# Kernel optimization log

Hardware: AMD Instinct MI355X
Metric: run time of the kernel (lower is better)

The kernel has to match this reference:

```python
import jax, jax.numpy as jnp
import numpy as np

H, HKV, HD = 16, 4, 128
EPS = 1.1920928955078125e-07  # float32 eps, torch F.rms_norm default


def _rms_norm(t):
    return t * jax.lax.rsqrt(jnp.mean(t * t, axis=-1, keepdims=True) + EPS)


def _rope(t, cos, sin):
    # t: [B, T, h, HD]; cos/sin: [T, HD//2] -> broadcast [1, T, 1, HD//2]
    te, to = t[..., 0::2], t[..., 1::2]
    c = cos[None, :, None, :]
    s = sin[None, :, None, :]
    re = te * c - to * s
    ro = te * s + to * c
    return jnp.stack((re, ro), axis=-1).reshape(t.shape)


def setup_inputs() -> dict:
    key = jax.random.key(0)
    ks = jax.random.split(key, 5)
    B, T, C = 2, 2048, 2048
    return {
        "x": jax.random.normal(ks[0], (B, T, C), jnp.float32),
        "Wq": jax.random.normal(ks[1], (C, C), jnp.float32) * 0.02,
        "Wk": jax.random.normal(ks[2], (HKV * HD, C), jnp.float32) * 0.02,
        "Wv": jax.random.normal(ks[3], (HKV * HD, C), jnp.float32) * 0.02,
        "Wo": jax.random.normal(ks[4], (C, C), jnp.float32) * 0.02,
        "q_gain": jnp.full((H,), 5.0, jnp.float32),
    }


def reference(x, Wq, Wk, Wv, Wo, q_gain):
    B, T, C = x.shape
    q = (x @ Wq.T).reshape(B, T, H, HD)
    k = (x @ Wk.T).reshape(B, T, HKV, HD)
    v = (x @ Wv.T).reshape(B, T, HKV, HD)

    q = _rms_norm(q)
    k = _rms_norm(k)

    theta = 1.0 / (10000.0 ** (jnp.arange(0, HD, 2, dtype=jnp.float32) / HD))
    t = jnp.arange(T, dtype=jnp.float32)
    freqs = jnp.outer(t, theta)  # [T, HD//2]
    cos, sin = jnp.cos(freqs), jnp.sin(freqs)

    q = _rope(q, cos, sin)
    k = _rope(k, cos, sin)
    q = q * q_gain[None, None, :, None]

    qh = q.transpose(0, 2, 1, 3)                       # [B, H, T, HD]
    kh = jnp.repeat(k.transpose(0, 2, 1, 3), H // HKV, axis=1)
    vh = jnp.repeat(v.transpose(0, 2, 1, 3), H // HKV, axis=1)

    scale = 1.0 / jnp.sqrt(jnp.float32(HD))
    scores = jnp.einsum("bhqd,bhkd->bhqk", qh, kh) * scale
    causal = jnp.tril(jnp.ones((T, T), bool))
    scores = jnp.where(causal[None, None], scores, jnp.finfo(scores.dtype).min)
    attn = jax.nn.softmax(scores, axis=-1)
    out = jnp.einsum("bhqk,bhkd->bhqd", attn, vh)
    out = out.transpose(0, 2, 1, 3).reshape(B, T, C)
    return out @ Wo.T
```

## Files before the change

kernel.cpp:

```cpp
#include <hip/hip_runtime.h>
#include <hip/hip_bf16.h>

#define TSEQ 2048
#define CDIM 2048
#define NH   16
#define NKV  4
#define HDIM 128
#define BATCH 2
#define MROWS (BATCH*TSEQ)
#define KVC   (NKV*HDIM)
#define QKVC  (CDIM + 2*KVC)

typedef short bf16x8 __attribute__((ext_vector_type(8)));
typedef float f32x4  __attribute__((ext_vector_type(4)));

typedef const __attribute__((address_space(1))) void* gptr_t;
typedef __attribute__((address_space(3))) void* sptr_t;

__device__ inline void async16(const __hip_bfloat16* g, __hip_bfloat16* l) {
  __builtin_amdgcn_global_load_lds((gptr_t)g, (sptr_t)l, 16, 0, 0);
}

__device__ inline f32x4 mfma16(bf16x8 a, bf16x8 b, f32x4 c) {
  return __builtin_amdgcn_mfma_f32_16x16x32_bf16(a, b, c, 0, 0, 0);
}

__device__ inline float bfbits2f(unsigned short u) {
  return __uint_as_float(((unsigned)u) << 16);
}

__device__ inline unsigned short f2bfu(float x) {
  __hip_bfloat16 t = __float2bfloat16(x);
  return *(unsigned short*)&t;
}

__device__ inline int swz128(int row, int col) {
  return row*128 + (((col >> 3) ^ (row & 15)) << 3) + (col & 7);
}
__device__ inline int swz64(int row, int col) {
  return row*64 + ((((col >> 3) ^ row) & 7) << 3) + (col & 7);
}

__global__ void canary(const void* __restrict__ x, int* __restrict__ flag) {
  __shared__ int cnt[256];
  int tid = threadIdx.x;
  const unsigned short* u = (const unsigned short*)x;
  int c = 0;
#pragma unroll
  for (int i = 0; i < 4; ++i) {
    float a = fabsf(bfbits2f(u[(tid*4 + i)*2]));
    if (a >= 1e-6f && a <= 1e3f) c++;
  }
  cnt[tid] = c;
  __syncthreads();
  for (int s = 128; s > 0; s >>= 1) {
    if (tid < s) cnt[tid] += cnt[tid + s];
    __syncthreads();
  }
  if (tid == 0) *flag = (cnt[0] > 512) ? 1 : 0;
}

__global__ __launch_bounds__(256) void canonize_all(
    const void* __restrict__ xs,  const void* __restrict__ wqs,
    const void* __restrict__ wks, const void* __restrict__ wvs,
    const void* __restrict__ wos, const void* __restrict__ gs,
    __hip_bfloat16* __restrict__ xd,
    __hip_bfloat16* __restrict__ wqkv,
    __hip_bfloat16* __restrict__ wod,
    __hip_bfloat16* __restrict__ gd,
    const int* __restrict__ flag)
{
  int blk = blockIdx.x;
  const void* src; __hip_bfloat16* dst; int base, n;
  if      (blk < 4096) { src = xs;  dst = xd;                base = blk;        n = MROWS*CDIM; }
  else if (blk < 6144) { src = wqs; dst = wqkv;              base = blk - 4096; n = CDIM*CDIM; }
  else if (blk < 6656) { src = wks; dst = wqkv + (size_t)CDIM*CDIM;            base = blk - 6144; n = KVC*CDIM; }
  else if (blk < 7168) { src = wvs; dst = wqkv + (size_t)(CDIM+KVC)*CDIM;      base = blk - 6656; n = KVC*CDIM; }
  else if (blk < 9216) { src = wos; dst = wod;               base = blk - 7168; n = CDIM*CDIM; }
  else                 { src = gs;  dst = gd;                base = 0;          n = NH; }
  int idx = base*2048 + threadIdx.x*8;
  if (idx >= n) return;
  if (*flag) {
    *(bf16x8*)&dst[idx] = *(const bf16x8*)((const __hip_bfloat16*)src + idx);
  } else {
    const float* s = (const float*)src + idx;
#pragma unroll
    for (int j = 0; j < 8; ++j) dst[idx + j] = __float2bfloat16(s[j]);
  }
}

#define BK 64

__global__ __launch_bounds__(512, 2) void gemm_bt256(
    const __hip_bfloat16* __restrict__ A,
    const __hip_bfloat16* __restrict__ B,
    __hip_bfloat16* __restrict__ C,
    int M, int N, int K, int lda)
{
  __shared__ __align__(16) __hip_bfloat16 As[2][256*BK];
  __shared__ __align__(16) __hip_bfloat16 Bs[2][192*BK];
  const int tid  = threadIdx.x;
  const int wave = tid >> 6;
  const int lane = tid & 63;
  const int qd   = lane >> 4;
  const int ln   = lane & 15;
  const int m0   = blockIdx.y * 256;
  const int n0   = blockIdx.x * 192;
  const int wm   = (wave >> 2) * 128;
  const int wn   = (wave & 3) * 48;

  auto stageA = [&](int buf, int kt) {
    const __hip_bfloat16* src = A + (size_t)m0*lda + kt*BK;
    __hip_bfloat16* dst = &As[buf][0];
#pragma unroll
    for (int i = 0; i < 4; ++i) {
      int c = i*512 + tid;
      int row = c >> 3, sl = c & 7;
      int gs = sl ^ (row & 7);
      async16(&src[(size_t)row*lda + gs*8], &dst[(i*512 + wave*64)*8]);
    }
  };
  auto stageB = [&](int buf, int kt) {
    const __hip_bfloat16* src = B + (size_t)n0*K + kt*BK;
    __hip_bfloat16* dst = &Bs[buf][0];
#pragma unroll
    for (int i = 0; i < 3; ++i) {
      int c = i*512 + tid;
      int row = c >> 3, sl = c & 7;
      int gs = sl ^ (row & 7);
      async16(&src[(size_t)row*K + gs*8], &dst[(i*512 + wave*64)*8]);
    }
  };
  auto ldA = [&](int buf, int m, int kk) -> bf16x8 {
    int row = wm + m*16 + ln;
    return *(const bf16x8*)&As[buf][row*BK + (((kk*4 + qd) ^ (row & 7)) << 3)];
  };
  auto ldB = [&](int buf, int n, int kk) -> bf16x8 {
    int row = wn + n*16 + ln;
    return *(const bf16x8*)&Bs[buf][row*BK + (((kk*4 + qd) ^ (row & 7)) << 3)];
  };

  f32x4 acc[8][3] = {};
  const int nt = K / BK;

  stageA(0, 0); stageB(0, 0);
  if (nt > 1) {
    stageA(1, 1); stageB(1, 1);
    asm volatile("s_waitcnt vmcnt(7)" ::: "memory");
  } else {
    asm volatile("s_waitcnt vmcnt(0)" ::: "memory");
  }
  __builtin_amdgcn_s_barrier();

#pragma unroll 1
  for (int t = 0; t < nt; ++t) {
    const int buf = t & 1;
    bf16x8 a03[4][2], a47[4][2], b01[2][2], b2[2];

#pragma unroll
    for (int m = 0; m < 4; ++m)
#pragma unroll
      for (int kk = 0; kk < 2; ++kk) a03[m][kk] = ldA(buf, m, kk);
#pragma unroll
    for (int n = 0; n < 2; ++n)
#pragma unroll
      for (int kk = 0; kk < 2; ++kk) b01[n][kk] = ldB(buf, n, kk);
    __builtin_amdgcn_s_setprio(1);
#pragma unroll
    for (int m = 0; m < 4; ++m)
#pragma unroll
      for (int n = 0; n < 2; ++n)
#pragma unroll
        for (int kk = 0; kk < 2; ++kk)
          acc[m][n] = mfma16(a03[m][kk], b01[n][kk], acc[m][n]);
    __builtin_amdgcn_s_setprio(0);
    __builtin_amdgcn_s_barrier();

#pragma unroll
    for (int m = 0; m < 4; ++m)
#pragma unroll
      for (int kk = 0; kk < 2; ++kk) a47[m][kk] = ldA(buf, 4 + m, kk);
    __builtin_amdgcn_s_setprio(1);
#pragma unroll
    for (int m = 0; m < 4; ++m)
#pragma unroll
      for (int n = 0; n < 2; ++n)
#pragma unroll
        for (int kk = 0; kk < 2; ++kk)
          acc[4 + m][n] = mfma16(a47[m][kk], b01[n][kk], acc[4 + m][n]);
    __builtin_amdgcn_s_setprio(0);
    __builtin_amdgcn_s_barrier();

#pragma unroll
    for (int kk = 0; kk < 2; ++kk) b2[kk] = ldB(buf, 2, kk);
    if (t + 2 < nt) stageA(buf, t + 2);
    __builtin_amdgcn_s_setprio(1);
#pragma unroll
    for (int m = 0; m < 4; ++m)
#pragma unroll
      for (int kk = 0; kk < 2; ++kk)
        acc[m][2] = mfma16(a03[m][kk], b2[kk], acc[m][2]);
    __builtin_amdgcn_s_setprio(0);
    __builtin_amdgcn_s_barrier();

    if (t + 2 < nt) stageB(buf, t + 2);
    __builtin_amdgcn_s_setprio(1);
#pragma unroll
    for (int m = 0; m < 4; ++m)
#pragma unroll
      for (int kk = 0; kk < 2; ++kk)
        acc[4 + m][2] = mfma16(a47[m][kk], b2[kk], acc[4 + m][2]);
    __builtin_amdgcn_s_setprio(0);
    if (t + 2 < nt) asm volatile("s_waitcnt vmcnt(7)" ::: "memory");
    else            asm volatile("s_waitcnt vmcnt(0)" ::: "memory");
    __builtin_amdgcn_s_barrier();
  }

#pragma unroll
  for (int m = 0; m < 8; ++m)
#pragma unroll
    for (int n = 0; n < 3; ++n) {
      int row = m0 + wm + m*16 + qd*4;
      int col = n0 + wn + n*16 + ln;
#pragma unroll
      for (int r = 0; r < 4; ++r)
        C[(size_t)(row + r)*N + col] = __float2bfloat16(acc[m][n][r]);
    }
}

__global__ __launch_bounds__(512, 2) void gemm_out(
    const __hip_bfloat16* __restrict__ A,
    const __hip_bfloat16* __restrict__ B,
    void* __restrict__ C,
    int M, int N, int K, int lda, const int* __restrict__ flag)
{
  __shared__ __align__(16) __hip_bfloat16 As[2][128*BK];
  __shared__ __align__(16) __hip_bfloat16 Bs[2][256*BK];
  const int tid  = threadIdx.x;
  const int wave = tid >> 6;
  const int lane = tid & 63;
  const int qd   = lane >> 4;
  const int ln   = lane & 15;
  const int m0   = blockIdx.y * 128;
  const int n0   = blockIdx.x * 256;
  const int wm   = (wave >> 2) * 64;
  const int wn   = (wave & 3) * 64;

  auto stageA = [&](int buf, int kt) {
    const __hip_bfloat16* src = A + (size_t)m0*lda + kt*BK;
    __hip_bfloat16* dst = &As[buf][0];
#pragma unroll
    for (int i = 0; i < 2; ++i) {
      int c = i*512 + tid;
      int row = c >> 3, sl = c & 7;
      int gs = sl ^ (row & 7);
      async16(&src[(size_t)row*lda + gs*8], &dst[(i*512 + wave*64)*8]);
    }
  };
  auto stageB = [&](int buf, int kt) {
    const __hip_bfloat16* src = B + (size_t)n0*K + kt*BK;
    __hip_bfloat16* dst = &Bs[buf][0];
#pragma unroll
    for (int i = 0; i < 4; ++i) {
      int c = i*512 + tid;
      int row = c >> 3, sl = c & 7;
      int gs = sl ^ (row & 7);
      async16(&src[(size_t)row*K + gs*8], &dst[(i*512 + wave*64)*8]);
    }
  };
  auto ldA = [&](int buf, int m, int kk) -> bf16x8 {
    int row = wm + m*16 + ln;
    return *(const bf16x8*)&As[buf][row*BK + (((kk*4 + qd) ^ (row & 7)) << 3)];
  };
  auto ldB = [&](int buf, int n, int kk) -> bf16x8 {
    int row = wn + n*16 + ln;
    return *(const bf16x8*)&Bs[buf][row*BK + (((kk*4 + qd) ^ (row & 7)) << 3)];
  };

  f32x4 acc[4][4] = {};
  const int nt = K / BK;

  stageA(0, 0); stageB(0, 0);
  if (nt > 1) {
    stageA(1, 1); stageB(1, 1);
    asm volatile("s_waitcnt vmcnt(6)" ::: "memory");
  } else {
    asm volatile("s_waitcnt vmcnt(0)" ::: "memory");
  }
  __builtin_amdgcn_s_barrier();

#pragma unroll 1
  for (int t = 0; t < nt; ++t) {
    const int buf = t & 1;
    bf16x8 a01[2][2], a23[2][2], b01[2][2], b23[2][2];

#pragma unroll
    for (int m = 0; m < 2; ++m)
#pragma unroll
      for (int kk = 0; kk < 2; ++kk) a01[m][kk] = ldA(buf, m, kk);
#pragma unroll
    for (int n = 0; n < 2; ++n)
#pragma unroll
      for (int kk = 0; kk < 2; ++kk) b01[n][kk] = ldB(buf, n, kk);
    __builtin_amdgcn_s_setprio(1);
#pragma unroll
    for (int m = 0; m < 2; ++m)
#pragma unroll
      for (int n = 0; n < 2; ++n)
#pragma unroll
        for (int kk = 0; kk < 2; ++kk)
          acc[m][n] = mfma16(a01[m][kk], b01[n][kk], acc[m][n]);
    __builtin_amdgcn_s_setprio(0);
    __builtin_amdgcn_s_barrier();

#pragma unroll
    for (int m = 0; m < 2; ++m)
#pragma unroll
      for (int kk = 0; kk < 2; ++kk) a23[m][kk] = ldA(buf, 2 + m, kk);
    __builtin_amdgcn_s_setprio(1);
#pragma unroll
    for (int m = 0; m < 2; ++m)
#pragma unroll
      for (int n = 0; n < 2; ++n)
#pragma unroll
        for (int kk = 0; kk < 2; ++kk)
          acc[2 + m][n] = mfma16(a23[m][kk], b01[n][kk], acc[2 + m][n]);
    __builtin_amdgcn_s_setprio(0);
    __builtin_amdgcn_s_barrier();

#pragma unroll
    for (int n = 0; n < 2; ++n)
#pragma unroll
      for (int kk = 0; kk < 2; ++kk) b23[n][kk] = ldB(buf, 2 + n, kk);
    if (t + 2 < nt) stageA(buf, t + 2);
    __builtin_amdgcn_s_setprio(1);
#pragma unroll
    for (int m = 0; m < 2; ++m)
#pragma unroll
      for (int n = 0; n < 2; ++n)
#pragma unroll
        for (int kk = 0; kk < 2; ++kk)
          acc[m][2 + n] = mfma16(a01[m][kk], b23[n][kk], acc[m][2 + n]);
    __builtin_amdgcn_s_setprio(0);
    __builtin_amdgcn_s_barrier();

    if (t + 2 < nt) stageB(buf, t + 2);
    __builtin_amdgcn_s_setprio(1);
#pragma unroll
    for (int m = 0; m < 2; ++m)
#pragma unroll
      for (int n = 0; n < 2; ++n)
#pragma unroll
        for (int kk = 0; kk < 2; ++kk)
          acc[2 + m][2 + n] = mfma16(a23[m][kk], b23[n][kk], acc[2 + m][2 + n]);
    __builtin_amdgcn_s_setprio(0);
    if (t + 2 < nt) asm volatile("s_waitcnt vmcnt(6)" ::: "memory");
    else            asm volatile("s_waitcnt vmcnt(0)" ::: "memory");
    __builtin_amdgcn_s_barrier();
  }

  const bool isbf = (*flag != 0);
#pragma unroll
  for (int m = 0; m < 4; ++m)
#pragma unroll
    for (int n = 0; n < 4; ++n) {
      int row = m0 + wm + m*16 + qd*4;
      int col = n0 + wn + n*16 + ln;
#pragma unroll
      for (int r = 0; r < 4; ++r) {
        if (isbf) ((__hip_bfloat16*)C)[(size_t)(row + r)*N + col] = __float2bfloat16(acc[m][n][r]);
        else      ((float*)C)[(size_t)(row + r)*N + col] = acc[m][n][r];
      }
    }
}

__global__ __launch_bounds__(256) void prep_qk(
    __hip_bfloat16* __restrict__ qkv,
    const __hip_bfloat16* __restrict__ gain)
{
  int wid  = blockIdx.x * 4 + (threadIdx.x >> 6);
  int lane = threadIdx.x & 63;
  bool isq = wid < MROWS*NH;
  int m, h;
  __hip_bfloat16* p;
  if (isq) { m = wid >> 4; h = wid & 15; p = qkv + (size_t)m*QKVC + h*HDIM; }
  else     { int w2 = wid - MROWS*NH; m = w2 >> 2; h = w2 & 3; p = qkv + (size_t)m*QKVC + CDIM + h*HDIM; }

  ushort2 raw = *(const ushort2*)((const unsigned short*)p + 2*lane);
  float e = bfbits2f(raw.x), o = bfbits2f(raw.y);
  float ss = e*e + o*o;
#pragma unroll
  for (int off = 32; off >= 1; off >>= 1) ss += __shfl_xor(ss, off);
  float rms = rsqrtf(ss * (1.0f/128.0f) + 1.1920928955078125e-07f);
  e *= rms; o *= rms;

  float theta = exp2f(-(float)(2*lane) * (1.0f/128.0f) * 13.287712379549449f);
  int t = m & (TSEQ-1);
  float fr = (float)t * theta;
  float c = cosf(fr), s = sinf(fr);
  float re = e*c - o*s;
  float ro = e*s + o*c;

  if (isq) {
    float g = bfbits2f(*(const unsigned short*)&gain[h]) * 0.08838834764831845f;
    re *= g; ro *= g;
  }
  p[2*lane]   = __float2bfloat16(re);
  p[2*lane+1] = __float2bfloat16(ro);
}

__global__ __launch_bounds__(256) void transpose_v(
    const __hip_bfloat16* __restrict__ qkv, __hip_bfloat16* __restrict__ vt)
{
  __shared__ __hip_bfloat16 tile[32][34];
  int tx = threadIdx.x & 31;
  int ty = threadIdx.x >> 5;
  int r0 = blockIdx.x * 32;
  int c0 = blockIdx.y * 32;
#pragma unroll
  for (int i = 0; i < 4; ++i)
    tile[ty + i*8][tx] = qkv[(size_t)(r0 + ty + i*8)*QKVC + (CDIM + KVC) + c0 + tx];
  __syncthreads();
  int b = r0 >> 11;
  int t = r0 & (TSEQ-1);
  int hk = c0 >> 7;
  int d0 = c0 & (HDIM-1);
#pragma unroll
  for (int i = 0; i < 4; ++i) {
    int d = d0 + ty + i*8;
    vt[((size_t)((b*NKV + hk)*HDIM + d))*TSEQ + t + tx] = tile[tx][ty + i*8];
  }
}

__global__ __launch_bounds__(256, 2) void attn_kernel(
    const __hip_bfloat16* __restrict__ qkv,
    const __hip_bfloat16* __restrict__ vt,
    __hip_bfloat16* __restrict__ out)
{
  const int tid  = threadIdx.x;
  const int wave = tid >> 6;
  const int lane = tid & 63;
  const int qd = lane >> 4, ln = lane & 15;
  const int p  = blockIdx.x;
  const int h  = blockIdx.y;
  const int b  = blockIdx.z;
  const int hk = h >> 2;

  const __hip_bfloat16* K = qkv + (size_t)(b*TSEQ)*QKVC + CDIM + hk*HDIM;
  const __hip_bfloat16* V = vt + ((size_t)(b*NKV + hk)*HDIM)*TSEQ;

  __shared__ __align__(16) __hip_bfloat16 Ks[64*128];
  __shared__ __align__(16) __hip_bfloat16 Vs[128*64];
  __shared__ __align__(16) __hip_bfloat16 Pb[64*64];
  __shared__ float Lb[4][64];

  auto issueK = [&](int t0) {
#pragma unroll
    for (int i = 0; i < 4; ++i) {
      int c = i*256 + tid;
      int row = c >> 4, cc = c & 15;
      int gcc = cc ^ (row & 15);
      async16(&K[(size_t)(t0 + row)*QKVC + gcc*8], &Ks[(i*256 + wave*64)*8]);
    }
  };
  auto issueV = [&](int t0) {
#pragma unroll
    for (int i = 0; i < 4; ++i) {
      int c = i*256 + tid;
      int row = c >> 3, cc = c & 7;
      int gcc = cc ^ (row & 7);
      async16(&V[(size_t)row*TSEQ + t0 + gcc*8], &Vs[(i*256 + wave*64)*8]);
    }
  };

#pragma unroll 1
  for (int seg = 0; seg < 2; ++seg) {
    const int qt = seg ? (31 - p) : p;
    const int q0 = qt * 64;

    bf16x8 qfr[4][4];
#pragma unroll
    for (int qsub = 0; qsub < 4; ++qsub)
#pragma unroll
      for (int kc = 0; kc < 4; ++kc)
        qfr[qsub][kc] = *(const bf16x8*)&qkv[((size_t)(b*TSEQ + q0 + qsub*16 + ln))*QKVC + h*HDIM + kc*32 + qd*8];

    f32x4 o[2][4] = {};
    float lacc[4] = {0.f, 0.f, 0.f, 0.f};

    __syncthreads();
    issueK(0);
    __syncthreads();

#pragma unroll 1
    for (int kt = 0; kt <= qt; ++kt) {
      const int t0 = kt * 64;
      issueV(t0);

      f32x4 sc[4] = {};
#pragma unroll
      for (int kc = 0; kc < 4; ++kc) {
        bf16x8 kfa = *(const bf16x8*)&Ks[swz128(wave*16 + ln, kc*32 + qd*8)];
#pragma unroll
        for (int qsub = 0; qsub < 4; ++qsub)
          sc[qsub] = mfma16(kfa, qfr[qsub][kc], sc[qsub]);
      }
      if (kt == qt) {
#pragma unroll
        for (int qsub = 0; qsub < 4; ++qsub)
#pragma unroll
          for (int r = 0; r < 4; ++r) {
            int kv = t0 + wave*16 + qd*4 + r;
            int q  = q0 + qsub*16 + ln;
            if (kv > q) sc[qsub][r] = -1.0e30f;
          }
      }
#pragma unroll
      for (int qsub = 0; qsub < 4; ++qsub) {
#pragma unroll
        for (int r = 0; r < 4; ++r)
          sc[qsub][r] = __expf(sc[qsub][r]);
        lacc[qsub] += (sc[qsub][0] + sc[qsub][1]) + (sc[qsub][2] + sc[qsub][3]);
      }

#pragma unroll
      for (int qsub = 0; qsub < 4; ++qsub) {
        ushort4 pk;
        pk.x = f2bfu(sc[qsub][0]); pk.y = f2bfu(sc[qsub][1]);
        pk.z = f2bfu(sc[qsub][2]); pk.w = f2bfu(sc[qsub][3]);
        *(ushort4*)&Pb[swz64(qsub*16 + ln, wave*16 + qd*4)] = pk;
      }

      __syncthreads();
      if (kt < qt) issueK(t0 + 64);

      __builtin_amdgcn_s_setprio(1);
#pragma unroll
      for (int kc2 = 0; kc2 < 2; ++kc2) {
        bf16x8 pfb[4];
#pragma unroll
        for (int qsub = 0; qsub < 4; ++qsub)
          pfb[qsub] = *(const bf16x8*)&Pb[swz64(qsub*16 + ln, kc2*32 + qd*8)];
#pragma unroll
        for (int half = 0; half < 2; ++half) {
          bf16x8 vfa = *(const bf16x8*)&Vs[swz64(wave*32 + half*16 + ln, kc2*32 + qd*8)];
#pragma unroll
          for (int qsub = 0; qsub < 4; ++qsub)
            o[half][qsub] = mfma16(vfa, pfb[qsub], o[half][qsub]);
        }
      }
      __builtin_amdgcn_s_setprio(0);
      __syncthreads();
    }

#pragma unroll
    for (int qsub = 0; qsub < 4; ++qsub) {
      lacc[qsub] += __shfl_xor(lacc[qsub], 16);
      lacc[qsub] += __shfl_xor(lacc[qsub], 32);
    }
    if (qd == 0) {
#pragma unroll
      for (int qsub = 0; qsub < 4; ++qsub)
        Lb[wave][qsub*16 + ln] = lacc[qsub];
    }
    __syncthreads();
    float inv[4];
#pragma unroll
    for (int qsub = 0; qsub < 4; ++qsub) {
      int q = qsub*16 + ln;
      inv[qsub] = 1.0f / (((Lb[0][q] + Lb[1][q]) + (Lb[2][q] + Lb[3][q])));
    }

#pragma unroll
    for (int half = 0; half < 2; ++half)
#pragma unroll
      for (int qsub = 0; qsub < 4; ++qsub) {
        ushort4 pk;
        pk.x = f2bfu(o[half][qsub][0] * inv[qsub]);
        pk.y = f2bfu(o[half][qsub][1] * inv[qsub]);
        pk.z = f2bfu(o[half][qsub][2] * inv[qsub]);
        pk.w = f2bfu(o[half][qsub][3] * inv[qsub]);
        *(ushort4*)&Ks[swz128(qsub*16 + ln, wave*32 + half*16 + qd*4)] = pk;
      }
    __syncthreads();
#pragma unroll
    for (int pass = 0; pass < 4; ++pass) {
      int row = wave*16 + pass*4 + qd;
      bf16x8 val = *(const bf16x8*)&Ks[swz128(row, ln*8)];
      int q = q0 + row;
      *(bf16x8*)&out[((size_t)(b*TSEQ + q))*CDIM + h*HDIM + ln*8] = val;
    }
  }
}

extern "C" void kernel_launch(void* const* d_in, const int* in_sizes, int n_in,
                              void* d_out, int out_size, void* d_ws, size_t ws_size,
                              hipStream_t stream) {
  char* ws = (char*)d_ws;
  size_t off = 0;
  auto alloc = [&](size_t bytes) { char* p = ws + off; off += (bytes + 255) & ~(size_t)255; return p; };

  int* flag = (int*)alloc(256);
  __hip_bfloat16* xb   = (__hip_bfloat16*)alloc((size_t)MROWS*CDIM*2);
  __hip_bfloat16* wqkv = (__hip_bfloat16*)alloc((size_t)QKVC*CDIM*2);
  __hip_bfloat16* wob  = (__hip_bfloat16*)alloc((size_t)CDIM*CDIM*2);
  __hip_bfloat16* gb   = (__hip_bfloat16*)alloc(256);
  __hip_bfloat16* qkv  = (__hip_bfloat16*)alloc((size_t)MROWS*QKVC*2);
  __hip_bfloat16* vt   = (__hip_bfloat16*)alloc((size_t)MROWS*KVC*2);

  canary<<<1, 256, 0, stream>>>(d_in[0], flag);

  canonize_all<<<9217, 256, 0, stream>>>(
      d_in[0], d_in[1], d_in[2], d_in[3], d_in[4], d_in[5],
      xb, wqkv, wob, gb, flag);

  gemm_bt256<<<dim3(QKVC/192, MROWS/256), 512, 0, stream>>>(
      xb, wqkv, qkv, MROWS, QKVC, CDIM, CDIM);

  int nwaves = MROWS*NH + MROWS*NKV;
  prep_qk<<<nwaves/4, 256, 0, stream>>>(qkv, gb);

  transpose_v<<<dim3(MROWS/32, KVC/32), 256, 0, stream>>>(qkv, vt);

  attn_kernel<<<dim3(16, NH, BATCH), 256, 0, stream>>>(qkv, vt, xb);

  gemm_out<<<dim3(CDIM/256, MROWS/128), 512, 0, stream>>>(
      xb, wob, d_out, MROWS, CDIM, CDIM, CDIM, flag);
}
```

Baseline: 295.8 us.

## Prefetch next-tile LDS fragments across iterations and reshape output GEMM tile

Both GEMM kernels now load the first A/B register fragments for the next K-tile during the last MFMA phase of the current tile. This lets LDS reads overlap with matrix math instead of stalling at the top of each iteration, and the async global staging and waits are reordered to match. The output GEMM tile also changes from 128x256 to 256x128 with an 8x2 accumulator layout per wave, so each wave's A fragments are reused across the loop the same way as in the QKV GEMM. The cost is more live registers and tighter ordering assumptions around vmcnt/lgkmcnt waits and barriers.

Result: no change. 296.5 us (+0.2%).

```diff
diff --git a/kernel.cpp b/kernel.cpp
--- a/kernel.cpp
+++ b/kernel.cpp
@@ -152,19 +152,27 @@
   }
   __builtin_amdgcn_s_barrier();
 
+  bf16x8 a03[4][2], b01[2][2];
+#pragma unroll
+  for (int m = 0; m < 4; ++m)
+#pragma unroll
+    for (int kk = 0; kk < 2; ++kk) a03[m][kk] = ldA(0, m, kk);
+#pragma unroll
+  for (int n = 0; n < 2; ++n)
+#pragma unroll
+    for (int kk = 0; kk < 2; ++kk) b01[n][kk] = ldB(0, n, kk);
+
 #pragma unroll 1
   for (int t = 0; t < nt; ++t) {
     const int buf = t & 1;
-    bf16x8 a03[4][2], a47[4][2], b01[2][2], b2[2];
-
-#pragma unroll
-    for (int m = 0; m < 4; ++m)
-#pragma unroll
-      for (int kk = 0; kk < 2; ++kk) a03[m][kk] = ldA(buf, m, kk);
-#pragma unroll
-    for (int n = 0; n < 2; ++n)
-#pragma unroll
-      for (int kk = 0; kk < 2; ++kk) b01[n][kk] = ldB(buf, n, kk);
+    bf16x8 a47[4][2], b2[2];
+
+#pragma unroll
+    for (int m = 0; m < 4; ++m)
+#pragma unroll
+      for (int kk = 0; kk < 2; ++kk) a47[m][kk] = ldA(buf, 4 + m, kk);
+#pragma unroll
+    for (int kk = 0; kk < 2; ++kk) b2[kk] = ldB(buf, 2, kk);
     __builtin_amdgcn_s_setprio(1);
 #pragma unroll
     for (int m = 0; m < 4; ++m)
@@ -174,12 +182,10 @@
         for (int kk = 0; kk < 2; ++kk)
           acc[m][n] = mfma16(a03[m][kk], b01[n][kk], acc[m][n]);
     __builtin_amdgcn_s_setprio(0);
-    __builtin_amdgcn_s_barrier();
-
-#pragma unroll
-    for (int m = 0; m < 4; ++m)
-#pragma unroll
-      for (int kk = 0; kk < 2; ++kk) a47[m][kk] = ldA(buf, 4 + m, kk);
+    asm volatile("s_waitcnt lgkmcnt(0)" ::: "memory");
+    __builtin_amdgcn_s_barrier();
+
+    if (t + 2 < nt) stageA(buf, t + 2);
     __builtin_amdgcn_s_setprio(1);
 #pragma unroll
     for (int m = 0; m < 4; ++m)
@@ -191,9 +197,7 @@
     __builtin_amdgcn_s_setprio(0);
     __builtin_amdgcn_s_barrier();
 
-#pragma unroll
-    for (int kk = 0; kk < 2; ++kk) b2[kk] = ldB(buf, 2, kk);
-    if (t + 2 < nt) stageA(buf, t + 2);
+    if (t + 2 < nt) stageB(buf, t + 2);
     __builtin_amdgcn_s_setprio(1);
 #pragma unroll
     for (int m = 0; m < 4; ++m)
@@ -201,9 +205,20 @@
       for (int kk = 0; kk < 2; ++kk)
         acc[m][2] = mfma16(a03[m][kk], b2[kk], acc[m][2]);
     __builtin_amdgcn_s_setprio(0);
-    __builtin_amdgcn_s_barrier();
-
-    if (t + 2 < nt) stageB(buf, t + 2);
+    if (t + 2 < nt) asm volatile("s_waitcnt vmcnt(7)" ::: "memory");
+    else            asm volatile("s_waitcnt vmcnt(0)" ::: "memory");
+    __builtin_amdgcn_s_barrier();
+
+    if (t + 1 < nt) {
+#pragma unroll
+      for (int m = 0; m < 4; ++m)
+#pragma unroll
+        for (int kk = 0; kk < 2; ++kk) a03[m][kk] = ldA(buf ^ 1, m, kk);
+#pragma unroll
+      for (int n = 0; n < 2; ++n)
+#pragma unroll
+        for (int kk = 0; kk < 2; ++kk) b01[n][kk] = ldB(buf ^ 1, n, kk);
+    }
     __builtin_amdgcn_s_setprio(1);
 #pragma unroll
     for (int m = 0; m < 4; ++m)
@@ -211,8 +226,6 @@
       for (int kk = 0; kk < 2; ++kk)
         acc[4 + m][2] = mfma16(a47[m][kk], b2[kk], acc[4 + m][2]);
     __builtin_amdgcn_s_setprio(0);
-    if (t + 2 < nt) asm volatile("s_waitcnt vmcnt(7)" ::: "memory");
-    else            asm volatile("s_waitcnt vmcnt(0)" ::: "memory");
     __builtin_amdgcn_s_barrier();
   }
 
@@ -234,37 +247,37 @@
     void* __restrict__ C,
     int M, int N, int K, int lda, const int* __restrict__ flag)
 {
-  __shared__ __align__(16) __hip_bfloat16 As[2][128*BK];
-  __shared__ __align__(16) __hip_bfloat16 Bs[2][256*BK];
+  __shared__ __align__(16) __hip_bfloat16 As[2][256*BK];
+  __shared__ __align__(16) __hip_bfloat16 Bs[2][128*BK];
   const int tid  = threadIdx.x;
   const int wave = tid >> 6;
   const int lane = tid & 63;
   const int qd   = lane >> 4;
   const int ln   = lane & 15;
-  const int m0   = blockIdx.y * 128;
-  const int n0   = blockIdx.x * 256;
-  const int wm   = (wave >> 2) * 64;
-  const int wn   = (wave & 3) * 64;
+  const int m0   = blockIdx.y * 256;
+  const int n0   = blockIdx.x * 128;
+  const int wm   = (wave >> 2) * 128;
+  const int wn   = (wave & 3) * 32;
 
   auto stageA = [&](int buf, int kt) {
     const __hip_bfloat16* src = A + (size_t)m0*lda + kt*BK;
     __hip_bfloat16* dst = &As[buf][0];
+#pragma unroll
+    for (int i = 0; i < 4; ++i) {
+      int c = i*512 + tid;
+      int row = c >> 3, sl = c & 7;
+      int gs = sl ^ (row & 7);
+      async16(&src[(size_t)row*lda + gs*8], &dst[(i*512 + wave*64)*8]);
+    }
+  };
+  auto stageB = [&](int buf, int kt) {
+    const __hip_bfloat16* src = B + (size_t)n0*K + kt*BK;
+    __hip_bfloat16* dst = &Bs[buf][0];
 #pragma unroll
     for (int i = 0; i < 2; ++i) {
       int c = i*512 + tid;
       int row = c >> 3, sl = c & 7;
       int gs = sl ^ (row & 7);
-      async16(&src[(size_t)row*lda + gs*8], &dst[(i*512 + wave*64)*8]);
-    }
-  };
-  auto stageB = [&](int buf, int kt) {
-    const __hip_bfloat16* src = B + (size_t)n0*K + kt*BK;
-    __hip_bfloat16* dst = &Bs[buf][0];
-#pragma unroll
-    for (int i = 0; i < 4; ++i) {
-      int c = i*512 + tid;
-      int row = c >> 3, sl = c & 7;
-      int gs = sl ^ (row & 7);
       async16(&src[(size_t)row*K + gs*8], &dst[(i*512 + wave*64)*8]);
     }
   };
@@ -277,7 +290,7 @@
     return *(const bf16x8*)&Bs[buf][row*BK + (((kk*4 + qd) ^ (row & 7)) << 3)];
   };
 
-  f32x4 acc[4][4] = {};
+  f32x4 acc[8][2] = {};
   const int nt = K / BK;
 
   stageA(0, 0); stageB(0, 0);
@@ -289,81 +302,80 @@
   }
   __builtin_amdgcn_s_barrier();
 
+  bf16x8 a03[4][2], bn0[2];
+#pragma unroll
+  for (int m = 0; m < 4; ++m)
+#pragma unroll
+    for (int kk = 0; kk < 2; ++kk) a03[m][kk] = ldA(0, m, kk);
+#pragma unroll
+  for (int kk = 0; kk < 2; ++kk) bn0[kk] = ldB(0, 0, kk);
+
 #pragma unroll 1
   for (int t = 0; t < nt; ++t) {
     const int buf = t & 1;
-    bf16x8 a01[2][2], a23[2][2], b01[2][2], b23[2][2];
-
-#pragma unroll
-    for (int m = 0; m < 2; ++m)
-#pragma unroll
-      for (int kk = 0; kk < 2; ++kk) a01[m][kk] = ldA(buf, m, kk);
-#pragma unroll
-    for (int n = 0; n < 2; ++n)
-#pragma unroll
-      for (int kk = 0; kk < 2; ++kk) b01[n][kk] = ldB(buf, n, kk);
-    __builtin_amdgcn_s_setprio(1);
-#pragma unroll
-    for (int m = 0; m < 2; ++m)
-#pragma unroll
-      for (int n = 0; n < 2; ++n)
-#pragma unroll
-        for (int kk = 0; kk < 2; ++kk)
-          acc[m][n] = mfma16(a01[m][kk], b01[n][kk], acc[m][n]);
-    __builtin_amdgcn_s_setprio(0);
-    __builtin_amdgcn_s_barrier();
-
-#pragma unroll
-    for (int m = 0; m < 2; ++m)
-#pragma unroll
-      for (int kk = 0; kk < 2; ++kk) a23[m][kk] = ldA(buf, 2 + m, kk);
-    __builtin_amdgcn_s_setprio(1);
-#pragma unroll
-    for (int m = 0; m < 2; ++m)
-#pragma unroll
-      for (int n = 0; n < 2; ++n)
-#pragma unroll
-        for (int kk = 0; kk < 2; ++kk)
-          acc[2 + m][n] = mfma16(a23[m][kk], b01[n][kk], acc[2 + m][n]);
-    __builtin_amdgcn_s_setprio(0);
-    __builtin_amdgcn_s_barrier();
-
-#pragma unroll
-    for (int n = 0; n < 2; ++n)
-#pragma unroll
-      for (int kk = 0; kk < 2; ++kk) b23[n][kk] = ldB(buf, 2 + n, kk);
+    bf16x8 a47[4][2], bn1[2];
+
+#pragma unroll
+    for (int m = 0; m < 4; ++m)
+#pragma unroll
+      for (int kk = 0; kk < 2; ++kk) a47[m][kk] = ldA(buf, 4 + m, kk);
+#pragma unroll
+    for (int kk = 0; kk < 2; ++kk) bn1[kk] = ldB(buf, 1, kk);
+    __builtin_amdgcn_s_setprio(1);
+#pragma unroll
+    for (int m = 0; m < 4; ++m)
+#pragma unroll
+      for (int kk = 0; kk < 2; ++kk)
+        acc[m][0] = mfma16(a03[m][kk], bn0[kk], acc[m][0]);
+    __builtin_amdgcn_s_setprio(0);
+    asm volatile("s_waitcnt lgkmcnt(0)" ::: "memory");
+    __builtin_amdgcn_s_barrier();
+
     if (t + 2 < nt) stageA(buf, t + 2);
     __builtin_amdgcn_s_setprio(1);
 #pragma unroll
-    for (int m = 0; m < 2; ++m)
-#pragma unroll
-      for (int n = 0; n < 2; ++n)
-#pragma unroll
-        for (int kk = 0; kk < 2; ++kk)
-          acc[m][2 + n] = mfma16(a01[m][kk], b23[n][kk], acc[m][2 + n]);
+    for (int m = 0; m < 4; ++m)
+#pragma unroll
+      for (int kk = 0; kk < 2; ++kk)
+        acc[4 + m][0] = mfma16(a47[m][kk], bn0[kk], acc[4 + m][0]);
     __builtin_amdgcn_s_setprio(0);
     __builtin_amdgcn_s_barrier();
 
     if (t + 2 < nt) stageB(buf, t + 2);
     __builtin_amdgcn_s_setprio(1);
 #pragma unroll
-    for (int m = 0; m < 2; ++m)
-#pragma unroll
-      for (int n = 0; n < 2; ++n)
-#pragma unroll
-        for (int kk = 0; kk < 2; ++kk)
-          acc[2 + m][2 + n] = mfma16(a23[m][kk], b23[n][kk], acc[2 + m][2 + n]);
+    for (int m = 0; m < 4; ++m)
+#pragma unroll
+      for (int kk = 0; kk < 2; ++kk)
+        acc[m][1] = mfma16(a03[m][kk], bn1[kk], acc[m][1]);
     __builtin_amdgcn_s_setprio(0);
     if (t + 2 < nt) asm volatile("s_waitcnt vmcnt(6)" ::: "memory");
     else            asm volatile("s_waitcnt vmcnt(0)" ::: "memory");
     __builtin_amdgcn_s_barrier();
+
+    if (t + 1 < nt) {
+#pragma unroll
+      for (int m = 0; m < 4; ++m)
+#pragma unroll
+        for (int kk = 0; kk < 2; ++kk) a03[m][kk] = ldA(buf ^ 1, m, kk);
+#pragma unroll
+      for (int kk = 0; kk < 2; ++kk) bn0[kk] = ldB(buf ^ 1, 0, kk);
+    }
+    __builtin_amdgcn_s_setprio(1);
+#pragma unroll
+    for (int m = 0; m < 4; ++m)
+#pragma unroll
+      for (int kk = 0; kk < 2; ++kk)
+        acc[4 + m][1] = mfma16(a47[m][kk], bn1[kk], acc[4 + m][1]);
+    __builtin_amdgcn_s_setprio(0);
+    __builtin_amdgcn_s_barrier();
   }
 
   const bool isbf = (*flag != 0);
 #pragma unroll
-  for (int m = 0; m < 4; ++m)
-#pragma unroll
-    for (int n = 0; n < 4; ++n) {
+  for (int m = 0; m < 8; ++m)
+#pragma unroll
+    for (int n = 0; n < 2; ++n) {
       int row = m0 + wm + m*16 + qd*4;
       int col = n0 + wn + n*16 + ln;
 #pragma unroll
@@ -624,6 +636,6 @@
 
   attn_kernel<<<dim3(16, NH, BATCH), 256, 0, stream>>>(qkv, vt, xb);
 
-  gemm_out<<<dim3(CDIM/256, MROWS/128), 512, 0, stream>>>(
+  gemm_out<<<dim3(CDIM/128, MROWS/256), 512, 0, stream>>>(
       xb, wob, d_out, MROWS, CDIM, CDIM, CDIM, flag);
 }
```
